# Performance work log

Hardware: AMD Instinct MI355X
Metric: run time of the kernel (lower is better)

Reference implementation:

```python
import jax, jax.numpy as jnp
import numpy as np

N, E = 2048, 65536
EMBED, H0, H1 = 64, 128, 128
VOCAB = 625  # 5**k with k=4
SLOPE = 0.01  # F.leaky_relu_ default negative slope


def setup_inputs() -> dict:
    key = jax.random.key(0)
    ks = jax.random.split(key, 20)
    f = jax.random.normal
    return {
        "node_ids": jax.random.randint(ks[0], (N,), 0, VOCAB),
        "edge_index": jax.random.randint(ks[1], (2, E), 0, N),
        "edge_attr": jax.random.uniform(ks[2], (E, 1), dtype=jnp.float32),
        "m": (jax.random.uniform(ks[3], (N, N)) > 0.5).astype(jnp.float32),
        "emb": f(ks[4], (VOCAB, EMBED), dtype=jnp.float32) * 0.1,
        "l0_lin1": f(ks[5], (H0, EMBED + 1), dtype=jnp.float32) * 0.1,
        "l0_lin2": f(ks[6], (H0, H0), dtype=jnp.float32) * 0.1,
        "l0_att_l": f(ks[7], (H0,), dtype=jnp.float32) * 0.1,
        "l0_att_r": f(ks[8], (EMBED,), dtype=jnp.float32) * 0.1,
        "l0_bias": f(ks[9], (H0,), dtype=jnp.float32) * 0.1,
        "l1_lin1": f(ks[10], (H1, H0 + 1), dtype=jnp.float32) * 0.1,
        "l1_lin2": f(ks[11], (H1, H1), dtype=jnp.float32) * 0.1,
        "l1_att_l": f(ks[12], (H1,), dtype=jnp.float32) * 0.1,
        "l1_att_r": f(ks[13], (H0,), dtype=jnp.float32) * 0.1,
        "l1_bias": f(ks[14], (H1,), dtype=jnp.float32) * 0.1,
        "W1": f(ks[15], (20, (EMBED + H0 + H1) * 2), dtype=jnp.float32) * 0.1,
        "b1": f(ks[16], (20,), dtype=jnp.float32) * 0.1,
        "W2": f(ks[17], (20,), dtype=jnp.float32) * 0.1,
        "b2": f(ks[18], (1,), dtype=jnp.float32) * 0.1,
    }


def _segment_softmax(alpha, index, n):
    # numerically-stable softmax over edges grouped by destination node
    amax = jax.ops.segment_max(alpha, index, num_segments=n)
    amax = jnp.where(jnp.isfinite(amax), amax, 0.0)
    e = jnp.exp(alpha - amax[index])
    denom = jax.ops.segment_sum(e, index, num_segments=n)
    return e / (denom[index] + 1e-16)


def _gate_conv(x, src, dst, edge_attr, lin1, lin2, att_l, att_r, bias, n):
    # PyG AttentiveFP GATEConv: message = lin2(leaky_relu(lin1([x_j, e]))) * alpha
    h = jax.nn.leaky_relu(jnp.concatenate([x[src], edge_attr], axis=-1) @ lin1.T, SLOPE)  # [E,out]
    alpha = jax.nn.leaky_relu(h @ att_l + x[dst] @ att_r, SLOPE)  # [E]
    alpha = _segment_softmax(alpha, dst, n)
    msg = (h @ lin2.T) * alpha[:, None]
    return jax.ops.segment_sum(msg, dst, num_segments=n) + bias


def reference(node_ids, edge_index, edge_attr, m, emb,
              l0_lin1, l0_lin2, l0_att_l, l0_att_r, l0_bias,
              l1_lin1, l1_lin2, l1_att_l, l1_att_r, l1_bias,
              W1, b1, W2, b2):
    src, dst = edge_index[0], edge_index[1]
    x = emb[node_ids]  # [N, EMBED]
    h1 = jax.nn.relu(_gate_conv(x, src, dst, edge_attr, l0_lin1, l0_lin2, l0_att_l, l0_att_r, l0_bias, N))
    h2 = jax.nn.relu(_gate_conv(h1, src, dst, edge_attr, l1_lin1, l1_lin2, l1_att_l, l1_att_r, l1_bias, N))
    feat = jnp.concatenate([x, h1, h2], axis=-1)  # [N, C], C = EMBED+H0+H1
    C = feat.shape[-1]
    # 1x1 conv over concat([x_i, x_j]) == split linear: out[c,i,j] = W1[c,:C]@feat[i] + W1[c,C:]@feat[j] + b1[c]
    a = feat @ W1[:, :C].T  # [N, 20] row (i) term
    b = feat @ W1[:, C:].T  # [N, 20] col (j) term
    h = jax.nn.relu(a[:, None, :] + b[None, :, :] + b1)  # [N, N, 20]
    logits = (h @ W2 + b2[0]) * m  # [N, N]; mask multiplies logits as in original
    return jax.nn.softmax(logits, axis=1)
```

## Files before the change

kernel.cpp:

```cpp
#include <hip/hip_runtime.h>
#include <math.h>

#define N 2048
#define E 65536
#define EMBED 64
#define H 128
#define NT 20
#define C3 320
#define CAP 96
#define SLOPE 0.01f
#define NBLK 256
#define NTHR 512

__device__ __forceinline__ float leaky(float x) { return x > 0.f ? x : SLOPE * x; }

__device__ __forceinline__ float wave_sum(float v) {
#pragma unroll
    for (int o = 32; o > 0; o >>= 1) v += __shfl_xor(v, o, 64);
    return v;
}

__device__ __forceinline__ void grid_sync(int* ctr, int target, int b) {
    __syncthreads();
    if (threadIdx.x == 0) {
        __builtin_amdgcn_fence(__ATOMIC_RELEASE, "agent");
        __hip_atomic_fetch_add(&ctr[(b & 7) << 6], 1, __ATOMIC_RELAXED,
                               __HIP_MEMORY_SCOPE_AGENT);
        for (;;) {
            int sum = 0;
#pragma unroll
            for (int i = 0; i < 8; i++)
                sum += __hip_atomic_load(&ctr[i << 6], __ATOMIC_RELAXED,
                                         __HIP_MEMORY_SCOPE_AGENT);
            if (sum >= target) break;
            __builtin_amdgcn_s_sleep(32);
        }
        __builtin_amdgcn_fence(__ATOMIC_ACQUIRE, "agent");
    }
    __syncthreads();
}

__device__ __forceinline__ void gate_wave16(
    int base, int lane, float xr,
    const float* __restrict__ A,
    float w0, float w1, float attl0, float attl1,
    const int2* __restrict__ se, int cnt,
    float& out0, float& out1) {
    int c0 = 2 * lane;
    float mmax = -INFINITY, s = 0.f, v0 = 0.f, v1 = 0.f;
    for (int i0 = 0; i0 < cnt; i0 += 16) {
        int nb = cnt - i0; if (nb > 16) nb = 16;
        float h0[16], h1v[16], p[16];
#pragma unroll
        for (int e = 0; e < 16; e++) {
            float ea = 0.f; float2 av = make_float2(0.f, 0.f);
            if (e < nb) {
                int2 v = se[base + i0 + e];
                ea = __int_as_float(v.y);
                av = *(const float2*)&A[v.x * H + c0];
            }
            h0[e] = leaky(fmaf(w0, ea, av.x));
            h1v[e] = leaky(fmaf(w1, ea, av.y));
            p[e] = h0[e] * attl0 + h1v[e] * attl1;
        }
#pragma unroll
        for (int o = 32; o > 0; o >>= 1) {
#pragma unroll
            for (int e = 0; e < 16; e++) p[e] += __shfl_xor(p[e], o, 64);
        }
        float alpha[16];
#pragma unroll
        for (int e = 0; e < 16; e++)
            alpha[e] = (e < nb) ? leaky(p[e] + xr) : -INFINITY;
        float mb = alpha[0];
#pragma unroll
        for (int e = 1; e < 16; e++) mb = fmaxf(mb, alpha[e]);
        float mnew = fmaxf(mmax, mb);
        float scale = __expf(mmax - mnew);
        float sw = 0.f, sv0 = 0.f, sv1 = 0.f;
#pragma unroll
        for (int e = 0; e < 16; e++) {
            float we = __expf(alpha[e] - mnew);
            sw += we;
            sv0 = fmaf(we, h0[e], sv0);
            sv1 = fmaf(we, h1v[e], sv1);
        }
        s = fmaf(s, scale, sw);
        v0 = fmaf(v0, scale, sv0);
        v1 = fmaf(v1, scale, sv1);
        mmax = mnew;
    }
    float inv = 1.f / (s + 1e-16f);
    out0 = v0 * inv;
    out1 = v1 * inv;
}

__global__ __launch_bounds__(NTHR) void k_fused(
    const int* __restrict__ ids, const int* __restrict__ ei,
    const float* __restrict__ eattr, const float* __restrict__ mmat,
    const float* __restrict__ emb,
    const float* __restrict__ l0_lin1, const float* __restrict__ l0_lin2,
    const float* __restrict__ l0_att_l, const float* __restrict__ l0_att_r,
    const float* __restrict__ l0_bias,
    const float* __restrict__ l1_lin1, const float* __restrict__ l1_lin2,
    const float* __restrict__ l1_att_l, const float* __restrict__ l1_att_r,
    const float* __restrict__ l1_bias,
    const float* __restrict__ W1, const float* __restrict__ b1,
    const float* __restrict__ W2, const float* __restrict__ b2,
    int* __restrict__ cursor, int* __restrict__ bar,
    int2* __restrict__ se,
    float* __restrict__ A0, float* __restrict__ A1,
    float* __restrict__ bT,
    float* __restrict__ WT1, float* __restrict__ LT0, float* __restrict__ LT1,
    float* __restrict__ out) {
    __shared__ float smem[512 + 1024 + 1024 + 2560 + 160 + 16384 + 64 + 64];
    float* xL   = smem;
    float* agg  = smem + 512;
    float* hs   = smem + 1536;
    float* feat = smem + 2560;
    float* aL   = smem + 5120;
    float* Lrow = smem + 5280;
    float* redM = smem + 21664;
    float* redS = smem + 21728;
    const int b = blockIdx.x;
    const int tid = threadIdx.x;
    const int gtid = b * NTHR + tid;
    const int n0 = b * 8;

    if (gtid < E) {
        int d = ei[E + gtid];
        int pos = atomicAdd(&cursor[d], 1);
        if (pos < CAP)
            se[d * CAP + pos] = make_int2(ei[gtid], __float_as_int(eattr[gtid]));
    } else {
        int j = gtid - E;
        if (j < 16384) {
            WT1[j] = l1_lin1[(j & 127) * (H + 1) + (j >> 7)];
        } else if (j < 32768) {
            int jj = j - 16384;
            LT0[jj] = l0_lin2[(jj & 127) * H + (jj >> 7)];
        } else if (j < 49152) {
            int jj = j - 32768;
            LT1[jj] = l1_lin2[(jj & 127) * H + (jj >> 7)];
        }
    }
    {
        int g = tid >> 6, c = tid & 63;
        xL[g * EMBED + c] = emb[ids[n0 + g] * EMBED + c];
    }
    __syncthreads();
    {
        int k = tid & 127, q = tid >> 7;
        const float* wr = l0_lin1 + k * (EMBED + 1);
        float accA = 0.f, accB = 0.f;
#pragma unroll 4
        for (int c = 0; c < EMBED; c++) {
            float w = wr[c];
            accA = fmaf(xL[q * EMBED + c], w, accA);
            accB = fmaf(xL[(q + 4) * EMBED + c], w, accB);
        }
        A0[(n0 + q) * H + k] = accA;
        A0[(n0 + q + 4) * H + k] = accB;
    }
    grid_sync(bar, NBLK, b);

    {
        int wv = __builtin_amdgcn_readfirstlane(tid >> 6);
        int lane = tid & 63;
        int c0 = 2 * lane;
        int dst = n0 + wv;

        float xr = wave_sum(xL[wv * EMBED + lane] * l0_att_r[lane]);
        float attl0 = l0_att_l[c0], attl1 = l0_att_l[c0 + 1];
        float w0 = l0_lin1[c0 * (EMBED + 1) + EMBED];
        float w1 = l0_lin1[(c0 + 1) * (EMBED + 1) + EMBED];
        int cnt = cursor[dst]; if (cnt > CAP) cnt = CAP;

        float o0, o1;
        gate_wave16(dst * CAP, lane, xr, A0, w0, w1, attl0, attl1, se, cnt, o0, o1);
        agg[wv * H + c0] = o0;
        agg[wv * H + c0 + 1] = o1;
        __syncthreads();

        int k = tid & 127, q = tid >> 7;
        float bk = l0_bias[k];
        float acc0 = bk, acc1 = bk;
#pragma unroll 2
        for (int ct = 0; ct < H / 4; ct++) {
            float u0 = LT0[(4 * ct + 0) * H + k];
            float u1 = LT0[(4 * ct + 1) * H + k];
            float u2 = LT0[(4 * ct + 2) * H + k];
            float u3 = LT0[(4 * ct + 3) * H + k];
            float4 f0 = *(const float4*)&agg[q * H + 4 * ct];
            float4 f1 = *(const float4*)&agg[(q + 4) * H + 4 * ct];
            acc0 = fmaf(f0.x, u0, acc0); acc0 = fmaf(f0.y, u1, acc0);
            acc0 = fmaf(f0.z, u2, acc0); acc0 = fmaf(f0.w, u3, acc0);
            acc1 = fmaf(f1.x, u0, acc1); acc1 = fmaf(f1.y, u1, acc1);
            acc1 = fmaf(f1.z, u2, acc1); acc1 = fmaf(f1.w, u3, acc1);
        }
        hs[q * H + k] = fmaxf(acc0, 0.f);
        hs[(q + 4) * H + k] = fmaxf(acc1, 0.f);
        __syncthreads();

        float a0 = 0.f, a1 = 0.f;
#pragma unroll 2
        for (int ct = 0; ct < H / 4; ct++) {
            float u0 = WT1[(4 * ct + 0) * H + k];
            float u1 = WT1[(4 * ct + 1) * H + k];
            float u2 = WT1[(4 * ct + 2) * H + k];
            float u3 = WT1[(4 * ct + 3) * H + k];
            float4 f0 = *(const float4*)&hs[q * H + 4 * ct];
            float4 f1 = *(const float4*)&hs[(q + 4) * H + 4 * ct];
            a0 = fmaf(f0.x, u0, a0); a0 = fmaf(f0.y, u1, a0);
            a0 = fmaf(f0.z, u2, a0); a0 = fmaf(f0.w, u3, a0);
            a1 = fmaf(f1.x, u0, a1); a1 = fmaf(f1.y, u1, a1);
            a1 = fmaf(f1.z, u2, a1); a1 = fmaf(f1.w, u3, a1);
        }
        A1[(n0 + q) * H + k] = a0;
        A1[(n0 + q + 4) * H + k] = a1;
    }
    grid_sync(bar, 2 * NBLK, b);

    {
        int wv = __builtin_amdgcn_readfirstlane(tid >> 6);
        int lane = tid & 63;
        int c0 = 2 * lane;
        int dst = n0 + wv;

        float xr = wave_sum(hs[wv * H + lane] * l1_att_r[lane] +
                            hs[wv * H + 64 + lane] * l1_att_r[64 + lane]);
        float attl0 = l1_att_l[c0], attl1 = l1_att_l[c0 + 1];
        float w0 = l1_lin1[c0 * (H + 1) + H];
        float w1 = l1_lin1[(c0 + 1) * (H + 1) + H];
        int cnt = cursor[dst]; if (cnt > CAP) cnt = CAP;

        float o0, o1;
        gate_wave16(dst * CAP, lane, xr, A1, w0, w1, attl0, attl1, se, cnt, o0, o1);
        agg[wv * H + c0] = o0;
        agg[wv * H + c0 + 1] = o1;

        for (int idx = tid; idx < 8 * EMBED; idx += NTHR) {
            int g = idx >> 6, c = idx & 63;
            feat[g * C3 + c] = xL[g * EMBED + c];
        }
        for (int idx = tid; idx < 8 * H; idx += NTHR) {
            int g = idx >> 7, c = idx & 127;
            feat[g * C3 + EMBED + c] = hs[g * H + c];
        }
        __syncthreads();

        int k = tid & 127, q = tid >> 7;
        float bk = l1_bias[k];
        float acc0 = bk, acc1 = bk;
#pragma unroll 2
        for (int ct = 0; ct < H / 4; ct++) {
            float u0 = LT1[(4 * ct + 0) * H + k];
            float u1 = LT1[(4 * ct + 1) * H + k];
            float u2 = LT1[(4 * ct + 2) * H + k];
            float u3 = LT1[(4 * ct + 3) * H + k];
            float4 f0 = *(const float4*)&agg[q * H + 4 * ct];
            float4 f1 = *(const float4*)&agg[(q + 4) * H + 4 * ct];
            acc0 = fmaf(f0.x, u0, acc0); acc0 = fmaf(f0.y, u1, acc0);
            acc0 = fmaf(f0.z, u2, acc0); acc0 = fmaf(f0.w, u3, acc0);
            acc1 = fmaf(f1.x, u0, acc1); acc1 = fmaf(f1.y, u1, acc1);
            acc1 = fmaf(f1.z, u2, acc1); acc1 = fmaf(f1.w, u3, acc1);
        }
        feat[q * C3 + EMBED + H + k] = fmaxf(acc0, 0.f);
        feat[(q + 4) * C3 + EMBED + H + k] = fmaxf(acc1, 0.f);
        __syncthreads();

        if (tid < 320) {
            int g = tid / 40, u = tid % 40;
            int t = u % 20, side = u / 20;
            const float* wrow = W1 + t * (2 * C3) + side * C3;
            float s = 0.f;
#pragma unroll 4
            for (int ct = 0; ct < C3 / 4; ct++) {
                float4 fv = *(const float4*)&feat[g * C3 + 4 * ct];
                float4 wv4 = *(const float4*)&wrow[4 * ct];
                s = fmaf(fv.x, wv4.x, s);
                s = fmaf(fv.y, wv4.y, s);
                s = fmaf(fv.z, wv4.z, s);
                s = fmaf(fv.w, wv4.w, s);
            }
            if (side == 0) aL[g * NT + t] = s + b1[t];
            else bT[t * N + (n0 + g)] = s;
        }
    }
    grid_sync(bar, 3 * NBLK, b);

    {
        int lane = tid & 63, wv = tid >> 6;
        int j = 4 * tid;
        float w2r[NT];
#pragma unroll
        for (int t = 0; t < NT; t++) w2r[t] = W2[t];
        float b2v = b2[0];
        float4 bt4[NT];
#pragma unroll
        for (int t = 0; t < NT; t++) bt4[t] = *(const float4*)&bT[t * N + j];

#pragma unroll
        for (int g = 0; g < 8; g++) {
            float4 s4 = make_float4(b2v, b2v, b2v, b2v);
#pragma unroll
            for (int t = 0; t < NT; t++) {
                float a = aL[g * NT + t];
                float w = w2r[t];
                s4.x = fmaf(fmaxf(a + bt4[t].x, 0.f), w, s4.x);
                s4.y = fmaf(fmaxf(a + bt4[t].y, 0.f), w, s4.y);
                s4.z = fmaf(fmaxf(a + bt4[t].z, 0.f), w, s4.z);
                s4.w = fmaf(fmaxf(a + bt4[t].w, 0.f), w, s4.w);
            }
            float4 mm = *(const float4*)&mmat[(size_t)(n0 + g) * N + j];
            s4.x *= mm.x; s4.y *= mm.y; s4.z *= mm.z; s4.w *= mm.w;
            *(float4*)&Lrow[g * 2048 + j] = s4;
            float tm = fmaxf(fmaxf(s4.x, s4.y), fmaxf(s4.z, s4.w));
#pragma unroll
            for (int o = 32; o > 0; o >>= 1) tm = fmaxf(tm, __shfl_xor(tm, o, 64));
            if (lane == 0) redM[g * 8 + wv] = tm;
        }
        __syncthreads();
        float mfin[8];
#pragma unroll
        for (int g = 0; g < 8; g++) {
            float m = redM[g * 8 + 0];
#pragma unroll
            for (int w = 1; w < 8; w++) m = fmaxf(m, redM[g * 8 + w]);
            mfin[g] = m;
        }
#pragma unroll
        for (int g = 0; g < 8; g++) {
            float4 v = *(const float4*)&Lrow[g * 2048 + j];
            float ts = __expf(v.x - mfin[g]) + __expf(v.y - mfin[g]) +
                       __expf(v.z - mfin[g]) + __expf(v.w - mfin[g]);
#pragma unroll
            for (int o = 32; o > 0; o >>= 1) ts += __shfl_xor(ts, o, 64);
            if (lane == 0) redS[g * 8 + wv] = ts;
        }
        __syncthreads();
#pragma unroll
        for (int g = 0; g < 8; g++) {
            float s = 0.f;
#pragma unroll
            for (int w = 0; w < 8; w++) s += redS[g * 8 + w];
            float inv = 1.f / s;
            float4 v = *(const float4*)&Lrow[g * 2048 + j];
            float4 o4;
            o4.x = __expf(v.x - mfin[g]) * inv;
            o4.y = __expf(v.y - mfin[g]) * inv;
            o4.z = __expf(v.z - mfin[g]) * inv;
            o4.w = __expf(v.w - mfin[g]) * inv;
            *(float4*)&out[(size_t)(n0 + g) * N + j] = o4;
        }
    }
}

extern "C" void kernel_launch(void* const* d_in, const int* in_sizes, int n_in,
                              void* d_out, int out_size, void* d_ws, size_t ws_size,
                              hipStream_t stream) {
    const int*   node_ids = (const int*)d_in[0];
    const int*   ei       = (const int*)d_in[1];
    const float* eattr    = (const float*)d_in[2];
    const float* mmat     = (const float*)d_in[3];
    const float* emb      = (const float*)d_in[4];
    const float* l0_lin1  = (const float*)d_in[5];
    const float* l0_lin2  = (const float*)d_in[6];
    const float* l0_att_l = (const float*)d_in[7];
    const float* l0_att_r = (const float*)d_in[8];
    const float* l0_bias  = (const float*)d_in[9];
    const float* l1_lin1  = (const float*)d_in[10];
    const float* l1_lin2  = (const float*)d_in[11];
    const float* l1_att_l = (const float*)d_in[12];
    const float* l1_att_r = (const float*)d_in[13];
    const float* l1_bias  = (const float*)d_in[14];
    const float* W1       = (const float*)d_in[15];
    const float* b1       = (const float*)d_in[16];
    const float* W2       = (const float*)d_in[17];
    const float* b2       = (const float*)d_in[18];
    float* out = (float*)d_out;

    char* w = (char*)d_ws;
    auto alloc = [&](size_t bytes) {
        char* p = w;
        w += (bytes + 255) & ~(size_t)255;
        return p;
    };
    int*   cursor = (int*)alloc((N + 512) * sizeof(int));
    int*   bar    = cursor + N;
    int2*  se     = (int2*)alloc(N * CAP * sizeof(int2));
    float* A0     = (float*)alloc(N * H * sizeof(float));
    float* A1     = (float*)alloc(N * H * sizeof(float));
    float* bT     = (float*)alloc(NT * N * sizeof(float));
    float* WT1    = (float*)alloc(H * H * sizeof(float));
    float* LT0    = (float*)alloc(H * H * sizeof(float));
    float* LT1    = (float*)alloc(H * H * sizeof(float));

    hipMemsetAsync(cursor, 0, (N + 512) * sizeof(int), stream);

    k_fused<<<NBLK, NTHR, 0, stream>>>(node_ids, ei, eattr, mmat, emb,
                                       l0_lin1, l0_lin2, l0_att_l, l0_att_r, l0_bias,
                                       l1_lin1, l1_lin2, l1_att_l, l1_att_r, l1_bias,
                                       W1, b1, W2, b2,
                                       cursor, bar, se, A0, A1,
                                       bT, WT1, LT0, LT1, out);
}
```

Measured before the change: 204.9 us.

## Use hierarchical grid barrier, spread edge bucketing across blocks, cache softmax exps

The grid barrier becomes two-level. Blocks increment one of 8 padded counters, and the last arriver on each counter bumps a single root counter that all blocks poll, replacing the poll of 8 lines. The edge-bucketing phase now gives each block 256 edges and 256 transpose elements instead of loading only the first 128 blocks, which spreads the atomics. The final softmax stores the exponentials in shared memory so they are not recomputed in the normalization pass, at the cost of an extra shared-memory write.

```diff
diff --git a/kernel.cpp b/kernel.cpp
--- a/kernel.cpp
+++ b/kernel.cpp
@@ -20,21 +20,16 @@
     return v;
 }
 
-__device__ __forceinline__ void grid_sync(int* ctr, int target, int b) {
+__device__ __forceinline__ void grid_sync(int* lines, int* root, int phase, int b) {
     __syncthreads();
     if (threadIdx.x == 0) {
         __builtin_amdgcn_fence(__ATOMIC_RELEASE, "agent");
-        __hip_atomic_fetch_add(&ctr[(b & 7) << 6], 1, __ATOMIC_RELAXED,
-                               __HIP_MEMORY_SCOPE_AGENT);
-        for (;;) {
-            int sum = 0;
-#pragma unroll
-            for (int i = 0; i < 8; i++)
-                sum += __hip_atomic_load(&ctr[i << 6], __ATOMIC_RELAXED,
-                                         __HIP_MEMORY_SCOPE_AGENT);
-            if (sum >= target) break;
-            __builtin_amdgcn_s_sleep(32);
-        }
+        int t = __hip_atomic_fetch_add(&lines[(b & 7) << 6], 1, __ATOMIC_RELAXED,
+                                       __HIP_MEMORY_SCOPE_AGENT);
+        if (t == 32 * phase - 1)
+            __hip_atomic_fetch_add(root, 1, __ATOMIC_RELAXED, __HIP_MEMORY_SCOPE_AGENT);
+        while (__hip_atomic_load(root, __ATOMIC_RELAXED, __HIP_MEMORY_SCOPE_AGENT) < 8 * phase)
+            __builtin_amdgcn_s_sleep(16);
         __builtin_amdgcn_fence(__ATOMIC_ACQUIRE, "agent");
     }
     __syncthreads();
@@ -107,7 +102,7 @@
     const float* __restrict__ l1_bias,
     const float* __restrict__ W1, const float* __restrict__ b1,
     const float* __restrict__ W2, const float* __restrict__ b2,
-    int* __restrict__ cursor, int* __restrict__ bar,
+    int* __restrict__ cursor, int* __restrict__ bar, int* __restrict__ root,
     int2* __restrict__ se,
     float* __restrict__ A0, float* __restrict__ A1,
     float* __restrict__ bT,
@@ -124,16 +119,16 @@
     float* redS = smem + 21728;
     const int b = blockIdx.x;
     const int tid = threadIdx.x;
-    const int gtid = b * NTHR + tid;
     const int n0 = b * 8;
 
-    if (gtid < E) {
-        int d = ei[E + gtid];
+    if (tid < 256) {
+        int e = b * 256 + tid;
+        int d = ei[E + e];
         int pos = atomicAdd(&cursor[d], 1);
         if (pos < CAP)
-            se[d * CAP + pos] = make_int2(ei[gtid], __float_as_int(eattr[gtid]));
+            se[d * CAP + pos] = make_int2(ei[e], __float_as_int(eattr[e]));
     } else {
-        int j = gtid - E;
+        int j = b * 256 + (tid - 256);
         if (j < 16384) {
             WT1[j] = l1_lin1[(j & 127) * (H + 1) + (j >> 7)];
         } else if (j < 32768) {
@@ -162,7 +157,7 @@
         A0[(n0 + q) * H + k] = accA;
         A0[(n0 + q + 4) * H + k] = accB;
     }
-    grid_sync(bar, NBLK, b);
+    grid_sync(bar, root, 1, b);
 
     {
         int wv = __builtin_amdgcn_readfirstlane(tid >> 6);
@@ -219,7 +214,7 @@
         A1[(n0 + q) * H + k] = a0;
         A1[(n0 + q + 4) * H + k] = a1;
     }
-    grid_sync(bar, 2 * NBLK, b);
+    grid_sync(bar, root, 2, b);
 
     {
         int wv = __builtin_amdgcn_readfirstlane(tid >> 6);
@@ -287,7 +282,7 @@
             else bT[t * N + (n0 + g)] = s;
         }
     }
-    grid_sync(bar, 3 * NBLK, b);
+    grid_sync(bar, root, 3, b);
 
     {
         int lane = tid & 63, wv = tid >> 6;
@@ -332,8 +327,12 @@
 #pragma unroll
         for (int g = 0; g < 8; g++) {
             float4 v = *(const float4*)&Lrow[g * 2048 + j];
-            float ts = __expf(v.x - mfin[g]) + __expf(v.y - mfin[g]) +
-                       __expf(v.z - mfin[g]) + __expf(v.w - mfin[g]);
+            v.x = __expf(v.x - mfin[g]);
+            v.y = __expf(v.y - mfin[g]);
+            v.z = __expf(v.z - mfin[g]);
+            v.w = __expf(v.w - mfin[g]);
+            *(float4*)&Lrow[g * 2048 + j] = v;
+            float ts = v.x + v.y + v.z + v.w;
 #pragma unroll
             for (int o = 32; o > 0; o >>= 1) ts += __shfl_xor(ts, o, 64);
             if (lane == 0) redS[g * 8 + wv] = ts;
@@ -346,12 +345,8 @@
             for (int w = 0; w < 8; w++) s += redS[g * 8 + w];
             float inv = 1.f / s;
             float4 v = *(const float4*)&Lrow[g * 2048 + j];
-            float4 o4;
-            o4.x = __expf(v.x - mfin[g]) * inv;
-            o4.y = __expf(v.y - mfin[g]) * inv;
-            o4.z = __expf(v.z - mfin[g]) * inv;
-            o4.w = __expf(v.w - mfin[g]) * inv;
-            *(float4*)&out[(size_t)(n0 + g) * N + j] = o4;
+            v.x *= inv; v.y *= inv; v.z *= inv; v.w *= inv;
+            *(float4*)&out[(size_t)(n0 + g) * N + j] = v;
         }
     }
 }
@@ -386,8 +381,9 @@
         w += (bytes + 255) & ~(size_t)255;
         return p;
     };
-    int*   cursor = (int*)alloc((N + 512) * sizeof(int));
+    int*   cursor = (int*)alloc((N + 640) * sizeof(int));
     int*   bar    = cursor + N;
+    int*   root   = bar + 512;
     int2*  se     = (int2*)alloc(N * CAP * sizeof(int2));
     float* A0     = (float*)alloc(N * H * sizeof(float));
     float* A1     = (float*)alloc(N * H * sizeof(float));
@@ -396,12 +392,12 @@
     float* LT0    = (float*)alloc(H * H * sizeof(float));
     float* LT1    = (float*)alloc(H * H * sizeof(float));
 
-    hipMemsetAsync(cursor, 0, (N + 512) * sizeof(int), stream);
+    hipMemsetAsync(cursor, 0, (N + 640) * sizeof(int), stream);
 
     k_fused<<<NBLK, NTHR, 0, stream>>>(node_ids, ei, eattr, mmat, emb,
                                        l0_lin1, l0_lin2, l0_att_l, l0_att_r, l0_bias,
                                        l1_lin1, l1_lin2, l1_att_l, l1_att_r, l1_bias,
                                        W1, b1, W2, b2,
-                                       cursor, bar, se, A0, A1,
+                                       cursor, bar, root, se, A0, A1,
                                        bT, WT1, LT0, LT1, out);
 }
```

After: 207.3 us. Within noise of the previous version (+1.2%).
